# Kernel optimization log

Measured on AMD Instinct MI355X. Metric: run time of the kernel, lower is better.

The kernel has to match this reference:

```python
import jax, jax.numpy as jnp
import numpy as np

# R-FCN PSRoI pooling constants (match init_kwargs)
P = 7          # pooled_height == pooled_width
GS = 7         # group_size
D = 21         # output_dim
SCALE = 0.0625 # spatial_scale (1/16)


def setup_inputs() -> dict:
    key = jax.random.key(0)
    k1, k2, k3, k4 = jax.random.split(key, 4)
    N, C, H, W = 4, D * GS * GS, 80, 80   # C = output_dim * group_size^2
    R = 2048
    features = jax.random.normal(k1, (N, C, H, W), dtype=jnp.float32)
    img = H / SCALE  # 1280 px image
    bidx = jax.random.randint(k2, (R,), 0, N).astype(jnp.float32)
    xy1 = jax.random.uniform(k3, (R, 2), minval=0.0, maxval=img * 0.6)
    wh = jax.random.uniform(k4, (R, 2), minval=img * 0.05, maxval=img * 0.4)
    xy2 = jnp.clip(xy1 + wh, 0.0, img - 1.0)
    rois = jnp.concatenate([bidx[:, None], xy1, xy2], axis=1)  # [R,5]: (b,x1,y1,x2,y2)
    return {"features": features, "rois": rois}


def reference(features, rois):
    """Position-sensitive RoI pooling (R-FCN psroi_pooling_forward_cuda semantics).

    Each output bin (ctop, ph, pw) averages feature channel
    c = (ctop*GS + gh)*GS + gw over the bin's integer pixel region.
    Bin sums are computed exactly via a 2D integral image, turning the
    irregular per-bin reduction into 4 gathers per bin.
    """
    N, C, H, W = features.shape
    R = rois.shape[0]

    # Integral image: ii[n,c,i,j] = sum of features[n,c,:i,:j]; shape [N,C,H+1,W+1]
    ii = jnp.pad(
        jnp.cumsum(jnp.cumsum(features, axis=2), axis=3),
        ((0, 0), (0, 0), (1, 0), (1, 0)),
    )

    b = rois[:, 0].astype(jnp.int32)                       # [R]
    x1 = jnp.round(rois[:, 1]) * SCALE
    y1 = jnp.round(rois[:, 2]) * SCALE
    x2 = (jnp.round(rois[:, 3]) + 1.0) * SCALE
    y2 = (jnp.round(rois[:, 4]) + 1.0) * SCALE
    bin_w = jnp.maximum(x2 - x1, 0.1) / P                  # [R]
    bin_h = jnp.maximum(y2 - y1, 0.1) / P

    g = jnp.arange(P, dtype=jnp.float32)                   # bin index grid
    hs = jnp.clip(jnp.floor(g[None, :] * bin_h[:, None] + y1[:, None]), 0, H).astype(jnp.int32)        # [R,P]
    he = jnp.clip(jnp.ceil((g[None, :] + 1.0) * bin_h[:, None] + y1[:, None]), 0, H).astype(jnp.int32)
    ws = jnp.clip(jnp.floor(g[None, :] * bin_w[:, None] + x1[:, None]), 0, W).astype(jnp.int32)
    we = jnp.clip(jnp.ceil((g[None, :] + 1.0) * bin_w[:, None] + x1[:, None]), 0, W).astype(jnp.int32)

    # Position-sensitive channel map: c[ctop,ph,pw] = (ctop*GS+gh)*GS+gw
    ctop = jnp.arange(D)[:, None, None]
    gh = jnp.clip((jnp.arange(P) * GS) // P, 0, GS - 1)[None, :, None]
    gw = jnp.clip((jnp.arange(P) * GS) // P, 0, GS - 1)[None, None, :]
    cmap = (ctop * GS + gh) * GS + gw                      # [D,P,P]

    # Broadcast gather indices to [R,D,P,P]
    B = b[:, None, None, None]
    Cc = cmap[None]
    HS = hs[:, None, :, None]; HE = he[:, None, :, None]
    WS = ws[:, None, None, :]; WE = we[:, None, None, :]

    s = ii[B, Cc, HE, WE] - ii[B, Cc, HS, WE] - ii[B, Cc, HE, WS] + ii[B, Cc, HS, WS]
    area = ((HE - HS) * (WE - WS)).astype(features.dtype)
    out = jnp.where(area > 0, s / jnp.maximum(area, 1.0), jnp.zeros((), features.dtype))
    return out  # [R, D, P, P]
```

## Files before the change

kernel.cpp:

```cpp
#include <hip/hip_runtime.h>

#define P   7
#define GS  7
#define D   21
#define HH  80
#define WW  80
#define CC  (D * GS * GS)
#define PLANE (HH * WW)
#define IW  81
#define NSEG 5
#define SEGLEN 16

__device__ __forceinline__ float recip7() {
    union { unsigned u; float f; } c; c.u = 0x3E124925u; return c.f;
}

__device__ __forceinline__ float mul_add_nofma(float a, float b, float c) {
    float t = a * b;
    asm volatile("" : "+v"(t));
    return t + c;
}

__global__ __launch_bounds__(1024) void prep_kernel(
    const float* __restrict__ rois, int R, int N,
    unsigned short* __restrict__ hshe,
    unsigned short* __restrict__ wswe,
    int* __restrict__ list, int* __restrict__ count)
{
    __shared__ unsigned char bsh[2048];
    int tid = threadIdx.x;

    for (int r = tid; r < R; r += 1024) {
        const float* roi = rois + (size_t)r * 5;
        bsh[r] = (unsigned char)(int)roi[0];

        float x1 = rintf(roi[1]) * 0.0625f;
        float y1 = rintf(roi[2]) * 0.0625f;
        float x2 = (rintf(roi[3]) + 1.0f) * 0.0625f;
        float y2 = (rintf(roi[4]) + 1.0f) * 0.0625f;
        float bin_w = fmaxf(x2 - x1, 0.1f) * recip7();
        float bin_h = fmaxf(y2 - y1, 0.1f) * recip7();
        asm volatile("" : "+v"(bin_w), "+v"(bin_h));

        #pragma unroll
        for (int g = 0; g < 7; ++g) {
            float hs_f = floorf(mul_add_nofma((float)g,       bin_h, y1));
            float he_f = ceilf (mul_add_nofma((float)(g + 1), bin_h, y1));
            float ws_f = floorf(mul_add_nofma((float)g,       bin_w, x1));
            float we_f = ceilf (mul_add_nofma((float)(g + 1), bin_w, x1));
            int hs = (int)fminf(fmaxf(hs_f, 0.0f), 80.0f);
            int he = (int)fminf(fmaxf(he_f, 0.0f), 80.0f);
            int ws = (int)fminf(fmaxf(ws_f, 0.0f), 80.0f);
            int we = (int)fminf(fmaxf(we_f, 0.0f), 80.0f);
            hshe[r * 7 + g] = (unsigned short)(hs | (he << 8));
            wswe[r * 7 + g] = (unsigned short)(ws | (we << 8));
        }
    }
    __syncthreads();

    int wave = tid >> 6, lane = tid & 63;
    if (wave < N) {
        int b = wave, offset = 0;
        for (int r0 = 0; r0 < R; r0 += 64) {
            int r = r0 + lane;
            bool m = (r < R) && (bsh[r] == (unsigned char)b);
            unsigned long long mask = __ballot(m);
            int pos = offset + __popcll(mask & ((1ull << lane) - 1ull));
            if (m) list[b * R + pos] = r;
            offset += __popcll(mask);
        }
        if (lane == 0) count[b] = offset;
    }
}

template <bool FAST>
__global__ __launch_bounds__(512) void psroi_plane_kernel(
    const float* __restrict__ feat,
    const float* __restrict__ rois, int R,
    const unsigned short* __restrict__ hshe,
    const unsigned short* __restrict__ wswe,
    const int* __restrict__ list, const int* __restrict__ count,
    float* __restrict__ dst)
{
    __shared__ float ii[IW * IW];
    __shared__ float tot[NSEG][HH];

    int tid = threadIdx.x;
    int bid = blockIdx.x;
    int b   = bid / CC;
    int c   = bid % CC;
    int rem = c % (GS * GS);
    int gh  = rem / GS;
    int gw  = rem % GS;

    const float4* src4 = (const float4*)(feat + ((size_t)b * CC + c) * PLANE);
    for (int i = tid; i < PLANE / 4; i += 512) {
        float4 v = src4[i];
        int h = i / 20;
        int w = (i % 20) * 4;
        float* p = &ii[(h + 1) * IW + (w + 1)];
        p[0] = v.x; p[1] = v.y; p[2] = v.z; p[3] = v.w;
    }
    if (tid < IW) { ii[tid] = 0.0f; ii[tid * IW] = 0.0f; }
    __syncthreads();

    bool act = tid < NSEG * WW;
    int seg = tid / WW;
    int lw  = tid % WW;
    float v[SEGLEN];
    {
        int col = lw + 1, h0 = seg * SEGLEN + 1;
        if (act) {
            float s = 0.0f;
            #pragma unroll
            for (int k = 0; k < SEGLEN; ++k) { v[k] = ii[(h0 + k) * IW + col]; s += v[k]; }
            tot[seg][lw] = s;
        }
        __syncthreads();
        if (act) {
            float off = 0.0f;
            #pragma unroll
            for (int j = 0; j < NSEG - 1; ++j) if (j < seg) off += tot[j][lw];
            float run = off;
            #pragma unroll
            for (int k = 0; k < SEGLEN; ++k) { run += v[k]; ii[(h0 + k) * IW + col] = run; }
        }
        __syncthreads();
    }
    {
        int row = lw + 1, w0 = seg * SEGLEN + 1;
        if (act) {
            float s = 0.0f;
            #pragma unroll
            for (int k = 0; k < SEGLEN; ++k) { v[k] = ii[row * IW + w0 + k]; s += v[k]; }
            tot[seg][lw] = s;
        }
        __syncthreads();
        if (act) {
            float off = 0.0f;
            #pragma unroll
            for (int j = 0; j < NSEG - 1; ++j) if (j < seg) off += tot[j][lw];
            float run = off;
            #pragma unroll
            for (int k = 0; k < SEGLEN; ++k) { run += v[k]; ii[row * IW + w0 + k] = run; }
        }
        __syncthreads();
    }

    if (FAST) {
        int cnt = count[b];
        const int* lst = list + b * R;
        for (int i = tid; i < cnt; i += 512) {
            int r  = lst[i];
            int hh = hshe[r * 7 + gh];
            int ww = wswe[r * 7 + gw];
            int hs = hh & 255, he = hh >> 8;
            int ws = ww & 255, we = ww >> 8;
            float s = ii[he * IW + we] - ii[hs * IW + we]
                    - ii[he * IW + ws] + ii[hs * IW + ws];
            int area = (he - hs) * (we - ws);
            dst[(size_t)c * R + r] = (area > 0) ? (s / (float)area) : 0.0f;
        }
    } else {
        for (int r = tid; r < R; r += 512) {
            const float* roi = rois + (size_t)r * 5;
            if ((int)roi[0] != b) continue;
            float x1 = rintf(roi[1]) * 0.0625f;
            float y1 = rintf(roi[2]) * 0.0625f;
            float x2 = (rintf(roi[3]) + 1.0f) * 0.0625f;
            float y2 = (rintf(roi[4]) + 1.0f) * 0.0625f;
            float bin_w = fmaxf(x2 - x1, 0.1f) * recip7();
            float bin_h = fmaxf(y2 - y1, 0.1f) * recip7();
            asm volatile("" : "+v"(bin_w), "+v"(bin_h));
            float hs_f = floorf(mul_add_nofma((float)gh,       bin_h, y1));
            float he_f = ceilf (mul_add_nofma((float)(gh + 1), bin_h, y1));
            float ws_f = floorf(mul_add_nofma((float)gw,       bin_w, x1));
            float we_f = ceilf (mul_add_nofma((float)(gw + 1), bin_w, x1));
            int hs = (int)fminf(fmaxf(hs_f, 0.0f), 80.0f);
            int he = (int)fminf(fmaxf(he_f, 0.0f), 80.0f);
            int ws = (int)fminf(fmaxf(ws_f, 0.0f), 80.0f);
            int we = (int)fminf(fmaxf(we_f, 0.0f), 80.0f);
            float s = ii[he * IW + we] - ii[hs * IW + we]
                    - ii[he * IW + ws] + ii[hs * IW + ws];
            int area = (he - hs) * (we - ws);
            dst[(size_t)r * CC + c] = (area > 0) ? (s / (float)area) : 0.0f;
        }
    }
}

__global__ __launch_bounds__(256) void transpose_kernel(
    const float* __restrict__ in, float* __restrict__ out, int R, int C)
{
    __shared__ float t[64][65];
    int r0 = blockIdx.x * 64;
    int c0 = blockIdx.y * 64;
    int tx = threadIdx.x;
    int ty = threadIdx.y;

    #pragma unroll
    for (int k0 = 0; k0 < 64; k0 += 4) {
        int k = k0 + ty;
        int cc = c0 + k, rr = r0 + tx;
        if (cc < C && rr < R) t[k][tx] = in[(size_t)cc * R + rr];
    }
    __syncthreads();
    #pragma unroll
    for (int k0 = 0; k0 < 64; k0 += 4) {
        int k = k0 + ty;
        int rr = r0 + k, cc = c0 + tx;
        if (rr < R && cc < C) out[(size_t)rr * C + cc] = t[tx][k];
    }
}

extern "C" void kernel_launch(void* const* d_in, const int* in_sizes, int n_in,
                              void* d_out, int out_size, void* d_ws, size_t ws_size,
                              hipStream_t stream)
{
    const float* feat = (const float*)d_in[0];
    const float* rois = (const float*)d_in[1];
    float* out        = (float*)d_out;

    int R = in_sizes[1] / 5;
    int N = in_sizes[0] / (CC * PLANE);

    size_t off_wsT  = 0;
    size_t off_hshe = (off_wsT + (size_t)CC * R * sizeof(float) + 15) & ~(size_t)15;
    size_t off_wswe = off_hshe + (size_t)R * 7 * sizeof(unsigned short);
    size_t off_list = (off_wswe + (size_t)R * 7 * sizeof(unsigned short) + 15) & ~(size_t)15;
    size_t off_cnt  = off_list + (size_t)N * R * sizeof(int);
    size_t need     = off_cnt + (size_t)N * sizeof(int);

    if (ws_size >= need && N <= 8 && R <= 2048) {
        char* ws = (char*)d_ws;
        float*          ws_T = (float*)(ws + off_wsT);
        unsigned short* hshe = (unsigned short*)(ws + off_hshe);
        unsigned short* wswe = (unsigned short*)(ws + off_wswe);
        int*            list = (int*)(ws + off_list);
        int*            cnt  = (int*)(ws + off_cnt);

        prep_kernel<<<1, 1024, 0, stream>>>(rois, R, N, hshe, wswe, list, cnt);
        psroi_plane_kernel<true><<<N * CC, 512, 0, stream>>>(
            feat, rois, R, hshe, wswe, list, cnt, ws_T);
        dim3 blk(64, 4), grd((R + 63) / 64, (CC + 63) / 64);
        transpose_kernel<<<grd, blk, 0, stream>>>(ws_T, out, R, CC);
    } else {
        psroi_plane_kernel<false><<<N * CC, 512, 0, stream>>>(
            feat, rois, R, nullptr, nullptr, nullptr, nullptr, out);
    }
}
```

Baseline: 52.47 us.

## Load feature planes via global_load_lds and precompute per-bin edge table

```diff
diff --git a/kernel.cpp b/kernel.cpp
--- a/kernel.cpp
+++ b/kernel.cpp
@@ -7,7 +7,8 @@
 #define WW  80
 #define CC  (D * GS * GS)
 #define PLANE (HH * WW)
-#define IW  81
+#define IW  84
+#define NCHUNK (HH * (IW / 4))
 #define NSEG 5
 #define SEGLEN 16
 
@@ -21,68 +22,80 @@
     return t + c;
 }
 
-__global__ __launch_bounds__(1024) void prep_kernel(
+__device__ __forceinline__ void gll16(const float* g, float* l) {
+    __builtin_amdgcn_global_load_lds(
+        (const __attribute__((address_space(1))) void*)g,
+        (__attribute__((address_space(3))) void*)l,
+        16, 0, 0);
+}
+
+__global__ __launch_bounds__(256) void edge_kernel(
+    const float* __restrict__ rois, int R, uint2* __restrict__ tab)
+{
+    int r = blockIdx.x * 256 + threadIdx.x;
+    if (r >= R) return;
+    const float* roi = rois + (size_t)r * 5;
+
+    float x1 = rintf(roi[1]) * 0.0625f;
+    float y1 = rintf(roi[2]) * 0.0625f;
+    float x2 = (rintf(roi[3]) + 1.0f) * 0.0625f;
+    float y2 = (rintf(roi[4]) + 1.0f) * 0.0625f;
+    float bin_w = fmaxf(x2 - x1, 0.1f) * recip7();
+    float bin_h = fmaxf(y2 - y1, 0.1f) * recip7();
+    asm volatile("" : "+v"(bin_w), "+v"(bin_h));
+
+    int hsA[7], heA[7], wsA[7], weA[7];
+    #pragma unroll
+    for (int g = 0; g < 7; ++g) {
+        float hs_f = floorf(mul_add_nofma((float)g,       bin_h, y1));
+        float he_f = ceilf (mul_add_nofma((float)(g + 1), bin_h, y1));
+        float ws_f = floorf(mul_add_nofma((float)g,       bin_w, x1));
+        float we_f = ceilf (mul_add_nofma((float)(g + 1), bin_w, x1));
+        hsA[g] = (int)fminf(fmaxf(hs_f, 0.0f), 80.0f);
+        heA[g] = (int)fminf(fmaxf(he_f, 0.0f), 80.0f);
+        wsA[g] = (int)fminf(fmaxf(ws_f, 0.0f), 80.0f);
+        weA[g] = (int)fminf(fmaxf(we_f, 0.0f), 80.0f);
+    }
+    uint2* t = tab + (size_t)r * 49;
+    #pragma unroll
+    for (int gh = 0; gh < 7; ++gh) {
+        #pragma unroll
+        for (int gw = 0; gw < 7; ++gw) {
+            int hs = hsA[gh], he = heA[gh], ws = wsA[gw], we = weA[gw];
+            int area = (he - hs) * (we - ws);
+            float rcp = (area > 0) ? (1.0f / (float)area) : 0.0f;
+            unsigned e = (unsigned)hs | ((unsigned)he << 8)
+                       | ((unsigned)ws << 16) | ((unsigned)we << 24);
+            t[gh * 7 + gw] = make_uint2(e, __float_as_uint(rcp));
+        }
+    }
+}
+
+__global__ __launch_bounds__(512) void compact_kernel(
     const float* __restrict__ rois, int R, int N,
-    unsigned short* __restrict__ hshe,
-    unsigned short* __restrict__ wswe,
     int* __restrict__ list, int* __restrict__ count)
 {
-    __shared__ unsigned char bsh[2048];
-    int tid = threadIdx.x;
-
-    for (int r = tid; r < R; r += 1024) {
-        const float* roi = rois + (size_t)r * 5;
-        bsh[r] = (unsigned char)(int)roi[0];
-
-        float x1 = rintf(roi[1]) * 0.0625f;
-        float y1 = rintf(roi[2]) * 0.0625f;
-        float x2 = (rintf(roi[3]) + 1.0f) * 0.0625f;
-        float y2 = (rintf(roi[4]) + 1.0f) * 0.0625f;
-        float bin_w = fmaxf(x2 - x1, 0.1f) * recip7();
-        float bin_h = fmaxf(y2 - y1, 0.1f) * recip7();
-        asm volatile("" : "+v"(bin_w), "+v"(bin_h));
-
-        #pragma unroll
-        for (int g = 0; g < 7; ++g) {
-            float hs_f = floorf(mul_add_nofma((float)g,       bin_h, y1));
-            float he_f = ceilf (mul_add_nofma((float)(g + 1), bin_h, y1));
-            float ws_f = floorf(mul_add_nofma((float)g,       bin_w, x1));
-            float we_f = ceilf (mul_add_nofma((float)(g + 1), bin_w, x1));
-            int hs = (int)fminf(fmaxf(hs_f, 0.0f), 80.0f);
-            int he = (int)fminf(fmaxf(he_f, 0.0f), 80.0f);
-            int ws = (int)fminf(fmaxf(ws_f, 0.0f), 80.0f);
-            int we = (int)fminf(fmaxf(we_f, 0.0f), 80.0f);
-            hshe[r * 7 + g] = (unsigned short)(hs | (he << 8));
-            wswe[r * 7 + g] = (unsigned short)(ws | (we << 8));
-        }
-    }
-    __syncthreads();
-
-    int wave = tid >> 6, lane = tid & 63;
-    if (wave < N) {
-        int b = wave, offset = 0;
-        for (int r0 = 0; r0 < R; r0 += 64) {
-            int r = r0 + lane;
-            bool m = (r < R) && (bsh[r] == (unsigned char)b);
-            unsigned long long mask = __ballot(m);
-            int pos = offset + __popcll(mask & ((1ull << lane) - 1ull));
-            if (m) list[b * R + pos] = r;
-            offset += __popcll(mask);
-        }
-        if (lane == 0) count[b] = offset;
-    }
-}
-
-template <bool FAST>
+    int wave = threadIdx.x >> 6, lane = threadIdx.x & 63;
+    if (wave >= N) return;
+    int b = wave, offset = 0;
+    for (int r0 = 0; r0 < R; r0 += 64) {
+        int r = r0 + lane;
+        bool m = (r < R) && ((int)rois[(size_t)r * 5] == b);
+        unsigned long long mask = __ballot(m);
+        int pos = offset + __popcll(mask & ((1ull << lane) - 1ull));
+        if (m) list[b * R + pos] = r;
+        offset += __popcll(mask);
+    }
+    if (lane == 0) count[b] = offset;
+}
+
 __global__ __launch_bounds__(512) void psroi_plane_kernel(
-    const float* __restrict__ feat,
-    const float* __restrict__ rois, int R,
-    const unsigned short* __restrict__ hshe,
-    const unsigned short* __restrict__ wswe,
+    const float* __restrict__ feat, int R,
+    const uint2* __restrict__ tab,
     const int* __restrict__ list, const int* __restrict__ count,
     float* __restrict__ dst)
 {
-    __shared__ float ii[IW * IW];
+    __shared__ float ii[HH * IW];
     __shared__ float tot[NSEG][HH];
 
     int tid = threadIdx.x;
@@ -90,30 +103,32 @@
     int b   = bid / CC;
     int c   = bid % CC;
     int rem = c % (GS * GS);
-    int gh  = rem / GS;
-    int gw  = rem % GS;
-
-    const float4* src4 = (const float4*)(feat + ((size_t)b * CC + c) * PLANE);
-    for (int i = tid; i < PLANE / 4; i += 512) {
-        float4 v = src4[i];
-        int h = i / 20;
-        int w = (i % 20) * 4;
-        float* p = &ii[(h + 1) * IW + (w + 1)];
-        p[0] = v.x; p[1] = v.y; p[2] = v.z; p[3] = v.w;
-    }
-    if (tid < IW) { ii[tid] = 0.0f; ii[tid * IW] = 0.0f; }
+
+    const float* plane = feat + ((size_t)b * CC + c) * PLANE;
+
+    int wid = tid >> 6, lane = tid & 63;
+    for (int q0 = wid * 64; q0 < NCHUNK; q0 += 512) {
+        int q = q0 + lane;
+        if (q < NCHUNK) {
+            int row = q / 21;
+            int c4  = q - row * 21;
+            const float* src = plane + row * WW + ((c4 < 20) ? c4 * 4 : 0);
+            gll16(src, &ii[q0 * 4]);
+        }
+    }
     __syncthreads();
 
     bool act = tid < NSEG * WW;
     int seg = tid / WW;
     int lw  = tid % WW;
     float v[SEGLEN];
+
     {
-        int col = lw + 1, h0 = seg * SEGLEN + 1;
+        int h0 = seg * SEGLEN;
         if (act) {
             float s = 0.0f;
             #pragma unroll
-            for (int k = 0; k < SEGLEN; ++k) { v[k] = ii[(h0 + k) * IW + col]; s += v[k]; }
+            for (int k = 0; k < SEGLEN; ++k) { v[k] = ii[(h0 + k) * IW + lw]; s += v[k]; }
             tot[seg][lw] = s;
         }
         __syncthreads();
@@ -123,16 +138,21 @@
             for (int j = 0; j < NSEG - 1; ++j) if (j < seg) off += tot[j][lw];
             float run = off;
             #pragma unroll
-            for (int k = 0; k < SEGLEN; ++k) { run += v[k]; ii[(h0 + k) * IW + col] = run; }
+            for (int k = 0; k < SEGLEN; ++k) { run += v[k]; ii[(h0 + k) * IW + lw] = run; }
         }
         __syncthreads();
     }
     {
-        int row = lw + 1, w0 = seg * SEGLEN + 1;
+        int w0 = seg * SEGLEN;
         if (act) {
+            float4* rp = (float4*)&ii[lw * IW + w0];
             float s = 0.0f;
             #pragma unroll
-            for (int k = 0; k < SEGLEN; ++k) { v[k] = ii[row * IW + w0 + k]; s += v[k]; }
+            for (int k4 = 0; k4 < SEGLEN / 4; ++k4) {
+                float4 f = rp[k4];
+                v[k4*4+0] = f.x; v[k4*4+1] = f.y; v[k4*4+2] = f.z; v[k4*4+3] = f.w;
+                s += f.x + f.y + f.z + f.w;
+            }
             tot[seg][lw] = s;
         }
         __syncthreads();
@@ -142,49 +162,84 @@
             for (int j = 0; j < NSEG - 1; ++j) if (j < seg) off += tot[j][lw];
             float run = off;
             #pragma unroll
-            for (int k = 0; k < SEGLEN; ++k) { run += v[k]; ii[row * IW + w0 + k] = run; }
+            for (int k = 0; k < SEGLEN; ++k) { run += v[k]; v[k] = run; }
+            float4* wp = (float4*)&ii[lw * IW + w0];
+            #pragma unroll
+            for (int k4 = 0; k4 < SEGLEN / 4; ++k4)
+                wp[k4] = make_float4(v[k4*4+0], v[k4*4+1], v[k4*4+2], v[k4*4+3]);
         }
         __syncthreads();
     }
 
-    if (FAST) {
-        int cnt = count[b];
-        const int* lst = list + b * R;
-        for (int i = tid; i < cnt; i += 512) {
-            int r  = lst[i];
-            int hh = hshe[r * 7 + gh];
-            int ww = wswe[r * 7 + gw];
-            int hs = hh & 255, he = hh >> 8;
-            int ws = ww & 255, we = ww >> 8;
-            float s = ii[he * IW + we] - ii[hs * IW + we]
-                    - ii[he * IW + ws] + ii[hs * IW + ws];
-            int area = (he - hs) * (we - ws);
-            dst[(size_t)c * R + r] = (area > 0) ? (s / (float)area) : 0.0f;
-        }
-    } else {
-        for (int r = tid; r < R; r += 512) {
-            const float* roi = rois + (size_t)r * 5;
-            if ((int)roi[0] != b) continue;
-            float x1 = rintf(roi[1]) * 0.0625f;
-            float y1 = rintf(roi[2]) * 0.0625f;
-            float x2 = (rintf(roi[3]) + 1.0f) * 0.0625f;
-            float y2 = (rintf(roi[4]) + 1.0f) * 0.0625f;
-            float bin_w = fmaxf(x2 - x1, 0.1f) * recip7();
-            float bin_h = fmaxf(y2 - y1, 0.1f) * recip7();
-            asm volatile("" : "+v"(bin_w), "+v"(bin_h));
-            float hs_f = floorf(mul_add_nofma((float)gh,       bin_h, y1));
-            float he_f = ceilf (mul_add_nofma((float)(gh + 1), bin_h, y1));
-            float ws_f = floorf(mul_add_nofma((float)gw,       bin_w, x1));
-            float we_f = ceilf (mul_add_nofma((float)(gw + 1), bin_w, x1));
-            int hs = (int)fminf(fmaxf(hs_f, 0.0f), 80.0f);
-            int he = (int)fminf(fmaxf(he_f, 0.0f), 80.0f);
-            int ws = (int)fminf(fmaxf(ws_f, 0.0f), 80.0f);
-            int we = (int)fminf(fmaxf(we_f, 0.0f), 80.0f);
-            float s = ii[he * IW + we] - ii[hs * IW + we]
-                    - ii[he * IW + ws] + ii[hs * IW + ws];
-            int area = (he - hs) * (we - ws);
-            dst[(size_t)r * CC + c] = (area > 0) ? (s / (float)area) : 0.0f;
-        }
+    int cnt = count[b];
+    const int* lst = list + b * R;
+    for (int i = tid; i < cnt; i += 512) {
+        int r = lst[i];
+        uint2 t = tab[(size_t)r * 49 + rem];
+        int hs =  t.x        & 255;
+        int he = (t.x >> 8)  & 255;
+        int ws = (t.x >> 16) & 255;
+        int we = (t.x >> 24) & 255;
+        float rcp = __uint_as_float(t.y);
+
+        int h1 = max(he - 1, 0), h0i = max(hs - 1, 0);
+        int w1 = max(we - 1, 0), w0i = max(ws - 1, 0);
+        float vHEWE = ii[h1  * IW + w1];
+        float vHSWE = ii[h0i * IW + w1];
+        float vHEWS = ii[h1  * IW + w0i];
+        float vHSWS = ii[h0i * IW + w0i];
+        float A = (he > 0 && we > 0) ? vHEWE : 0.0f;
+        float B = (hs > 0 && we > 0) ? vHSWE : 0.0f;
+        float Cv = (he > 0 && ws > 0) ? vHEWS : 0.0f;
+        float Dv = (hs > 0 && ws > 0) ? vHSWS : 0.0f;
+        float s = ((A - B) - Cv) + Dv;
+        dst[(size_t)c * R + r] = s * rcp;
+    }
+}
+
+__global__ __launch_bounds__(256) void psroi_fallback_kernel(
+    const float* __restrict__ feat, const float* __restrict__ rois,
+    int R, float* __restrict__ out)
+{
+    __shared__ float ii[81 * 81];
+    int bid = blockIdx.x;
+    int b = bid / CC, c = bid % CC;
+    int rem = c % 49, gh = rem / 7, gw = rem % 7;
+
+    const float* plane = feat + ((size_t)b * CC + c) * PLANE;
+    for (int i = threadIdx.x; i < PLANE; i += 256) {
+        int h = i / WW, w = i % WW;
+        ii[(h + 1) * 81 + (w + 1)] = plane[i];
+    }
+    for (int i = threadIdx.x; i < 81; i += 256) { ii[i] = 0.0f; ii[i * 81] = 0.0f; }
+    __syncthreads();
+    if (threadIdx.x < WW) {
+        int w = threadIdx.x + 1; float s = 0.0f;
+        for (int h = 1; h <= HH; ++h) { s += ii[h * 81 + w]; ii[h * 81 + w] = s; }
+    }
+    __syncthreads();
+    if (threadIdx.x < HH) {
+        int h = threadIdx.x + 1; float* row = &ii[h * 81]; float s = 0.0f;
+        for (int w = 1; w <= WW; ++w) { s += row[w]; row[w] = s; }
+    }
+    __syncthreads();
+    for (int r = threadIdx.x; r < R; r += 256) {
+        const float* roi = rois + (size_t)r * 5;
+        if ((int)roi[0] != b) continue;
+        float x1 = rintf(roi[1]) * 0.0625f;
+        float y1 = rintf(roi[2]) * 0.0625f;
+        float x2 = (rintf(roi[3]) + 1.0f) * 0.0625f;
+        float y2 = (rintf(roi[4]) + 1.0f) * 0.0625f;
+        float bw = fmaxf(x2 - x1, 0.1f) * recip7();
+        float bh = fmaxf(y2 - y1, 0.1f) * recip7();
+        asm volatile("" : "+v"(bw), "+v"(bh));
+        int hs = (int)fminf(fmaxf(floorf(mul_add_nofma((float)gh,     bh, y1)), 0.0f), 80.0f);
+        int he = (int)fminf(fmaxf(ceilf (mul_add_nofma((float)(gh+1), bh, y1)), 0.0f), 80.0f);
+        int ws = (int)fminf(fmaxf(floorf(mul_add_nofma((float)gw,     bw, x1)), 0.0f), 80.0f);
+        int we = (int)fminf(fmaxf(ceilf (mul_add_nofma((float)(gw+1), bw, x1)), 0.0f), 80.0f);
+        float s = ii[he * 81 + we] - ii[hs * 81 + we] - ii[he * 81 + ws] + ii[hs * 81 + ws];
+        int area = (he - hs) * (we - ws);
+        out[(size_t)r * CC + c] = (area > 0) ? (s / (float)area) : 0.0f;
     }
 }
 
@@ -194,8 +249,7 @@
     __shared__ float t[64][65];
     int r0 = blockIdx.x * 64;
     int c0 = blockIdx.y * 64;
-    int tx = threadIdx.x;
-    int ty = threadIdx.y;
+    int tx = threadIdx.x, ty = threadIdx.y;
 
     #pragma unroll
     for (int k0 = 0; k0 < 64; k0 += 4) {
@@ -224,27 +278,24 @@
     int N = in_sizes[0] / (CC * PLANE);
 
     size_t off_wsT  = 0;
-    size_t off_hshe = (off_wsT + (size_t)CC * R * sizeof(float) + 15) & ~(size_t)15;
-    size_t off_wswe = off_hshe + (size_t)R * 7 * sizeof(unsigned short);
-    size_t off_list = (off_wswe + (size_t)R * 7 * sizeof(unsigned short) + 15) & ~(size_t)15;
+    size_t off_tab  = (off_wsT + (size_t)CC * R * sizeof(float) + 15) & ~(size_t)15;
+    size_t off_list = (off_tab + (size_t)R * 49 * sizeof(uint2) + 15) & ~(size_t)15;
     size_t off_cnt  = off_list + (size_t)N * R * sizeof(int);
     size_t need     = off_cnt + (size_t)N * sizeof(int);
 
-    if (ws_size >= need && N <= 8 && R <= 2048) {
+    if (ws_size >= need && N <= 8 && R <= 65536) {
         char* ws = (char*)d_ws;
-        float*          ws_T = (float*)(ws + off_wsT);
-        unsigned short* hshe = (unsigned short*)(ws + off_hshe);
-        unsigned short* wswe = (unsigned short*)(ws + off_wswe);
-        int*            list = (int*)(ws + off_list);
-        int*            cnt  = (int*)(ws + off_cnt);
-
-        prep_kernel<<<1, 1024, 0, stream>>>(rois, R, N, hshe, wswe, list, cnt);
-        psroi_plane_kernel<true><<<N * CC, 512, 0, stream>>>(
-            feat, rois, R, hshe, wswe, list, cnt, ws_T);
+        float* ws_T = (float*)(ws + off_wsT);
+        uint2* tab  = (uint2*)(ws + off_tab);
+        int*   list = (int*)(ws + off_list);
+        int*   cnt  = (int*)(ws + off_cnt);
+
+        edge_kernel<<<(R + 255) / 256, 256, 0, stream>>>(rois, R, tab);
+        compact_kernel<<<1, 512, 0, stream>>>(rois, R, N, list, cnt);
+        psroi_plane_kernel<<<N * CC, 512, 0, stream>>>(feat, R, tab, list, cnt, ws_T);
         dim3 blk(64, 4), grd((R + 63) / 64, (CC + 63) / 64);
         transpose_kernel<<<grd, blk, 0, stream>>>(ws_T, out, R, CC);
     } else {
-        psroi_plane_kernel<false><<<N * CC, 512, 0, stream>>>(
-            feat, rois, R, nullptr, nullptr, nullptr, nullptr, out);
-    }
-}
+        psroi_fallback_kernel<<<N * CC, 256, 0, stream>>>(feat, rois, R, out);
+    }
+}
```

After: 61.50 us. 17.2% more time.

## Precompute per-bin packed edges and reciprocal area in a compacted ROI-ordered table

Applied to the files above, without the earlier changes.

```diff
diff --git a/kernel.cpp b/kernel.cpp
--- a/kernel.cpp
+++ b/kernel.cpp
@@ -21,65 +21,86 @@
     return t + c;
 }
 
-__global__ __launch_bounds__(1024) void prep_kernel(
+__global__ __launch_bounds__(512) void compact_kernel(
     const float* __restrict__ rois, int R, int N,
-    unsigned short* __restrict__ hshe,
-    unsigned short* __restrict__ wswe,
-    int* __restrict__ list, int* __restrict__ count)
-{
-    __shared__ unsigned char bsh[2048];
-    int tid = threadIdx.x;
-
-    for (int r = tid; r < R; r += 1024) {
-        const float* roi = rois + (size_t)r * 5;
-        bsh[r] = (unsigned char)(int)roi[0];
-
-        float x1 = rintf(roi[1]) * 0.0625f;
-        float y1 = rintf(roi[2]) * 0.0625f;
-        float x2 = (rintf(roi[3]) + 1.0f) * 0.0625f;
-        float y2 = (rintf(roi[4]) + 1.0f) * 0.0625f;
-        float bin_w = fmaxf(x2 - x1, 0.1f) * recip7();
-        float bin_h = fmaxf(y2 - y1, 0.1f) * recip7();
-        asm volatile("" : "+v"(bin_w), "+v"(bin_h));
-
-        #pragma unroll
-        for (int g = 0; g < 7; ++g) {
-            float hs_f = floorf(mul_add_nofma((float)g,       bin_h, y1));
-            float he_f = ceilf (mul_add_nofma((float)(g + 1), bin_h, y1));
-            float ws_f = floorf(mul_add_nofma((float)g,       bin_w, x1));
-            float we_f = ceilf (mul_add_nofma((float)(g + 1), bin_w, x1));
-            int hs = (int)fminf(fmaxf(hs_f, 0.0f), 80.0f);
-            int he = (int)fminf(fmaxf(he_f, 0.0f), 80.0f);
-            int ws = (int)fminf(fmaxf(ws_f, 0.0f), 80.0f);
-            int we = (int)fminf(fmaxf(we_f, 0.0f), 80.0f);
-            hshe[r * 7 + g] = (unsigned short)(hs | (he << 8));
-            wswe[r * 7 + g] = (unsigned short)(ws | (we << 8));
-        }
-    }
-    __syncthreads();
-
-    int wave = tid >> 6, lane = tid & 63;
+    int* __restrict__ jlist, int* __restrict__ base)
+{
+    __shared__ int cntS[8];
+    __shared__ int baseS[9];
+    int wave = threadIdx.x >> 6, lane = threadIdx.x & 63;
+
     if (wave < N) {
-        int b = wave, offset = 0;
+        int b = wave, cnt = 0;
         for (int r0 = 0; r0 < R; r0 += 64) {
             int r = r0 + lane;
-            bool m = (r < R) && (bsh[r] == (unsigned char)b);
+            bool m = (r < R) && ((int)rois[(size_t)r * 5] == b);
+            cnt += __popcll(__ballot(m));
+        }
+        if (lane == 0) cntS[b] = cnt;
+    }
+    __syncthreads();
+    if (threadIdx.x == 0) {
+        int acc = 0;
+        for (int b = 0; b < N; ++b) { baseS[b] = acc; acc += cntS[b]; }
+        baseS[N] = acc;
+    }
+    __syncthreads();
+    if (wave < N) {
+        int b = wave, off = baseS[b];
+        for (int r0 = 0; r0 < R; r0 += 64) {
+            int r = r0 + lane;
+            bool m = (r < R) && ((int)rois[(size_t)r * 5] == b);
             unsigned long long mask = __ballot(m);
-            int pos = offset + __popcll(mask & ((1ull << lane) - 1ull));
-            if (m) list[b * R + pos] = r;
-            offset += __popcll(mask);
-        }
-        if (lane == 0) count[b] = offset;
-    }
-}
-
-template <bool FAST>
+            int pos = off + __popcll(mask & ((1ull << lane) - 1ull));
+            if (m) jlist[pos] = r;
+            off += __popcll(mask);
+        }
+    }
+    if (threadIdx.x <= N) base[threadIdx.x] = baseS[threadIdx.x];
+}
+
+__global__ __launch_bounds__(256) void edge_kernel(
+    const float* __restrict__ rois, const int* __restrict__ jlist,
+    const int* __restrict__ base, int N, int R,
+    uint2* __restrict__ tab2)
+{
+    int t = blockIdx.x * 256 + threadIdx.x;
+    if (t >= 49 * R) return;
+    int rem = t / R;
+    int j   = t - rem * R;
+    if (j >= base[N]) return;
+    int gh = rem / 7, gw = rem % 7;
+    int r = jlist[j];
+
+    const float* roi = rois + (size_t)r * 5;
+    float x1 = rintf(roi[1]) * 0.0625f;
+    float y1 = rintf(roi[2]) * 0.0625f;
+    float x2 = (rintf(roi[3]) + 1.0f) * 0.0625f;
+    float y2 = (rintf(roi[4]) + 1.0f) * 0.0625f;
+    float bin_w = fmaxf(x2 - x1, 0.1f) * recip7();
+    float bin_h = fmaxf(y2 - y1, 0.1f) * recip7();
+    asm volatile("" : "+v"(bin_w), "+v"(bin_h));
+
+    float hs_f = floorf(mul_add_nofma((float)gh,       bin_h, y1));
+    float he_f = ceilf (mul_add_nofma((float)(gh + 1), bin_h, y1));
+    float ws_f = floorf(mul_add_nofma((float)gw,       bin_w, x1));
+    float we_f = ceilf (mul_add_nofma((float)(gw + 1), bin_w, x1));
+    int hs = (int)fminf(fmaxf(hs_f, 0.0f), 80.0f);
+    int he = (int)fminf(fmaxf(he_f, 0.0f), 80.0f);
+    int ws = (int)fminf(fmaxf(ws_f, 0.0f), 80.0f);
+    int we = (int)fminf(fmaxf(we_f, 0.0f), 80.0f);
+
+    int area = (he - hs) * (we - ws);
+    float rcp = (area > 0) ? (1.0f / (float)area) : 0.0f;
+    unsigned e = (unsigned)hs | ((unsigned)he << 8)
+               | ((unsigned)ws << 16) | ((unsigned)we << 24);
+    tab2[t] = make_uint2(e, __float_as_uint(rcp));
+}
+
 __global__ __launch_bounds__(512) void psroi_plane_kernel(
-    const float* __restrict__ feat,
-    const float* __restrict__ rois, int R,
-    const unsigned short* __restrict__ hshe,
-    const unsigned short* __restrict__ wswe,
-    const int* __restrict__ list, const int* __restrict__ count,
+    const float* __restrict__ feat, int R,
+    const uint2* __restrict__ tab2,
+    const int* __restrict__ jlist, const int* __restrict__ base,
     float* __restrict__ dst)
 {
     __shared__ float ii[IW * IW];
@@ -90,8 +111,6 @@
     int b   = bid / CC;
     int c   = bid % CC;
     int rem = c % (GS * GS);
-    int gh  = rem / GS;
-    int gw  = rem % GS;
 
     const float4* src4 = (const float4*)(feat + ((size_t)b * CC + c) * PLANE);
     for (int i = tid; i < PLANE / 4; i += 512) {
@@ -108,6 +127,7 @@
     int seg = tid / WW;
     int lw  = tid % WW;
     float v[SEGLEN];
+
     {
         int col = lw + 1, h0 = seg * SEGLEN + 1;
         if (act) {
@@ -120,7 +140,7 @@
         if (act) {
             float off = 0.0f;
             #pragma unroll
-            for (int j = 0; j < NSEG - 1; ++j) if (j < seg) off += tot[j][lw];
+            for (int jj = 0; jj < NSEG - 1; ++jj) if (jj < seg) off += tot[jj][lw];
             float run = off;
             #pragma unroll
             for (int k = 0; k < SEGLEN; ++k) { run += v[k]; ii[(h0 + k) * IW + col] = run; }
@@ -139,7 +159,7 @@
         if (act) {
             float off = 0.0f;
             #pragma unroll
-            for (int j = 0; j < NSEG - 1; ++j) if (j < seg) off += tot[j][lw];
+            for (int jj = 0; jj < NSEG - 1; ++jj) if (jj < seg) off += tot[jj][lw];
             float run = off;
             #pragma unroll
             for (int k = 0; k < SEGLEN; ++k) { run += v[k]; ii[row * IW + w0 + k] = run; }
@@ -147,44 +167,64 @@
         __syncthreads();
     }
 
-    if (FAST) {
-        int cnt = count[b];
-        const int* lst = list + b * R;
-        for (int i = tid; i < cnt; i += 512) {
-            int r  = lst[i];
-            int hh = hshe[r * 7 + gh];
-            int ww = wswe[r * 7 + gw];
-            int hs = hh & 255, he = hh >> 8;
-            int ws = ww & 255, we = ww >> 8;
-            float s = ii[he * IW + we] - ii[hs * IW + we]
-                    - ii[he * IW + ws] + ii[hs * IW + ws];
-            int area = (he - hs) * (we - ws);
-            dst[(size_t)c * R + r] = (area > 0) ? (s / (float)area) : 0.0f;
-        }
-    } else {
-        for (int r = tid; r < R; r += 512) {
-            const float* roi = rois + (size_t)r * 5;
-            if ((int)roi[0] != b) continue;
-            float x1 = rintf(roi[1]) * 0.0625f;
-            float y1 = rintf(roi[2]) * 0.0625f;
-            float x2 = (rintf(roi[3]) + 1.0f) * 0.0625f;
-            float y2 = (rintf(roi[4]) + 1.0f) * 0.0625f;
-            float bin_w = fmaxf(x2 - x1, 0.1f) * recip7();
-            float bin_h = fmaxf(y2 - y1, 0.1f) * recip7();
-            asm volatile("" : "+v"(bin_w), "+v"(bin_h));
-            float hs_f = floorf(mul_add_nofma((float)gh,       bin_h, y1));
-            float he_f = ceilf (mul_add_nofma((float)(gh + 1), bin_h, y1));
-            float ws_f = floorf(mul_add_nofma((float)gw,       bin_w, x1));
-            float we_f = ceilf (mul_add_nofma((float)(gw + 1), bin_w, x1));
-            int hs = (int)fminf(fmaxf(hs_f, 0.0f), 80.0f);
-            int he = (int)fminf(fmaxf(he_f, 0.0f), 80.0f);
-            int ws = (int)fminf(fmaxf(ws_f, 0.0f), 80.0f);
-            int we = (int)fminf(fmaxf(we_f, 0.0f), 80.0f);
-            float s = ii[he * IW + we] - ii[hs * IW + we]
-                    - ii[he * IW + ws] + ii[hs * IW + ws];
-            int area = (he - hs) * (we - ws);
-            dst[(size_t)r * CC + c] = (area > 0) ? (s / (float)area) : 0.0f;
-        }
+    int j0 = base[b], j1 = base[b + 1];
+    const uint2* tb = tab2 + (size_t)rem * R;
+    for (int j = j0 + tid; j < j1; j += 512) {
+        uint2 t = tb[j];
+        int r = jlist[j];
+        int hs =  t.x        & 255;
+        int he = (t.x >> 8)  & 255;
+        int ws = (t.x >> 16) & 255;
+        int we =  t.x >> 24;
+        float s = ((ii[he * IW + we] - ii[hs * IW + we])
+                 -  ii[he * IW + ws]) + ii[hs * IW + ws];
+        dst[(size_t)c * R + r] = s * __uint_as_float(t.y);
+    }
+}
+
+__global__ __launch_bounds__(256) void psroi_fallback_kernel(
+    const float* __restrict__ feat, const float* __restrict__ rois,
+    int R, float* __restrict__ out)
+{
+    __shared__ float ii[IW * IW];
+    int bid = blockIdx.x;
+    int b = bid / CC, c = bid % CC;
+    int rem = c % 49, gh = rem / 7, gw = rem % 7;
+
+    const float* plane = feat + ((size_t)b * CC + c) * PLANE;
+    for (int i = threadIdx.x; i < PLANE; i += 256) {
+        int h = i / WW, w = i % WW;
+        ii[(h + 1) * IW + (w + 1)] = plane[i];
+    }
+    for (int i = threadIdx.x; i < IW; i += 256) { ii[i] = 0.0f; ii[i * IW] = 0.0f; }
+    __syncthreads();
+    if (threadIdx.x < WW) {
+        int w = threadIdx.x + 1; float s = 0.0f;
+        for (int h = 1; h <= HH; ++h) { s += ii[h * IW + w]; ii[h * IW + w] = s; }
+    }
+    __syncthreads();
+    if (threadIdx.x < HH) {
+        int h = threadIdx.x + 1; float* row = &ii[h * IW]; float s = 0.0f;
+        for (int w = 1; w <= WW; ++w) { s += row[w]; row[w] = s; }
+    }
+    __syncthreads();
+    for (int r = threadIdx.x; r < R; r += 256) {
+        const float* roi = rois + (size_t)r * 5;
+        if ((int)roi[0] != b) continue;
+        float x1 = rintf(roi[1]) * 0.0625f;
+        float y1 = rintf(roi[2]) * 0.0625f;
+        float x2 = (rintf(roi[3]) + 1.0f) * 0.0625f;
+        float y2 = (rintf(roi[4]) + 1.0f) * 0.0625f;
+        float bw = fmaxf(x2 - x1, 0.1f) * recip7();
+        float bh = fmaxf(y2 - y1, 0.1f) * recip7();
+        asm volatile("" : "+v"(bw), "+v"(bh));
+        int hs = (int)fminf(fmaxf(floorf(mul_add_nofma((float)gh,     bh, y1)), 0.0f), 80.0f);
+        int he = (int)fminf(fmaxf(ceilf (mul_add_nofma((float)(gh+1), bh, y1)), 0.0f), 80.0f);
+        int ws = (int)fminf(fmaxf(floorf(mul_add_nofma((float)gw,     bw, x1)), 0.0f), 80.0f);
+        int we = (int)fminf(fmaxf(ceilf (mul_add_nofma((float)(gw+1), bw, x1)), 0.0f), 80.0f);
+        float s = ii[he * IW + we] - ii[hs * IW + we] - ii[he * IW + ws] + ii[hs * IW + ws];
+        int area = (he - hs) * (we - ws);
+        out[(size_t)r * CC + c] = (area > 0) ? (s / (float)area) : 0.0f;
     }
 }
 
@@ -194,8 +234,7 @@
     __shared__ float t[64][65];
     int r0 = blockIdx.x * 64;
     int c0 = blockIdx.y * 64;
-    int tx = threadIdx.x;
-    int ty = threadIdx.y;
+    int tx = threadIdx.x, ty = threadIdx.y;
 
     #pragma unroll
     for (int k0 = 0; k0 < 64; k0 += 4) {
@@ -224,27 +263,24 @@
     int N = in_sizes[0] / (CC * PLANE);
 
     size_t off_wsT  = 0;
-    size_t off_hshe = (off_wsT + (size_t)CC * R * sizeof(float) + 15) & ~(size_t)15;
-    size_t off_wswe = off_hshe + (size_t)R * 7 * sizeof(unsigned short);
-    size_t off_list = (off_wswe + (size_t)R * 7 * sizeof(unsigned short) + 15) & ~(size_t)15;
-    size_t off_cnt  = off_list + (size_t)N * R * sizeof(int);
-    size_t need     = off_cnt + (size_t)N * sizeof(int);
-
-    if (ws_size >= need && N <= 8 && R <= 2048) {
+    size_t off_tab  = (off_wsT + (size_t)CC * R * sizeof(float) + 15) & ~(size_t)15;
+    size_t off_jl   = (off_tab + (size_t)49 * R * sizeof(uint2) + 15) & ~(size_t)15;
+    size_t off_base = off_jl + (size_t)R * sizeof(int);
+    size_t need     = off_base + (size_t)(N + 1) * sizeof(int);
+
+    if (ws_size >= need && N <= 8 && R <= 65536) {
         char* ws = (char*)d_ws;
-        float*          ws_T = (float*)(ws + off_wsT);
-        unsigned short* hshe = (unsigned short*)(ws + off_hshe);
-        unsigned short* wswe = (unsigned short*)(ws + off_wswe);
-        int*            list = (int*)(ws + off_list);
-        int*            cnt  = (int*)(ws + off_cnt);
-
-        prep_kernel<<<1, 1024, 0, stream>>>(rois, R, N, hshe, wswe, list, cnt);
-        psroi_plane_kernel<true><<<N * CC, 512, 0, stream>>>(
-            feat, rois, R, hshe, wswe, list, cnt, ws_T);
+        float* ws_T = (float*)(ws + off_wsT);
+        uint2* tab2 = (uint2*)(ws + off_tab);
+        int*   jl   = (int*)(ws + off_jl);
+        int*   base = (int*)(ws + off_base);
+
+        compact_kernel<<<1, 512, 0, stream>>>(rois, R, N, jl, base);
+        edge_kernel<<<(49 * R + 255) / 256, 256, 0, stream>>>(rois, jl, base, N, R, tab2);
+        psroi_plane_kernel<<<N * CC, 512, 0, stream>>>(feat, R, tab2, jl, base, ws_T);
         dim3 blk(64, 4), grd((R + 63) / 64, (CC + 63) / 64);
         transpose_kernel<<<grd, blk, 0, stream>>>(ws_T, out, R, CC);
     } else {
-        psroi_plane_kernel<false><<<N * CC, 512, 0, stream>>>(
-            feat, rois, R, nullptr, nullptr, nullptr, nullptr, out);
-    }
-}
+        psroi_fallback_kernel<<<N * CC, 256, 0, stream>>>(feat, rois, R, out);
+    }
+}
```

Result: slower. 62.58 us (+19.3%).
